# Optimization experiments

Hardware: AMD Instinct MI355X
Metric: run time of the kernel (lower is better)

The kernel has to match this reference:

```python
import jax, jax.numpy as jnp
import numpy as np

DIM = 1024
D_STATE = 16
D_CONV = 4
EXPAND = 2
D_INNER = EXPAND * DIM          # 2048
DT_RANK = -(-DIM // 16)        # ceil(dim/16) = 64
BATCH = 2
SEQ = 1024


def activation_quant(x):
    # int8 fake-quant with STE, per-row scale (matches torch source incl. grad paths)
    scale = 127.0 / jnp.clip(jnp.max(jnp.abs(x), axis=-1, keepdims=True), 1e-5)
    s = x * scale
    q = jnp.clip(jnp.round(s), -128.0, 127.0)
    return (jax.lax.stop_gradient(q - s) + s) / scale


def weight_quant(w):
    # ternary quant {-1,0,1} with straight-through estimator (grad = identity)
    scale = jnp.clip(jnp.mean(jnp.abs(w)), 1e-5)
    wq = jnp.clip(jnp.round(w / scale), -1.0, 1.0)
    return w + jax.lax.stop_gradient(wq - w)


def bit_linear(x, w):
    # LayerNorm (no affine, eps=1e-5) -> act quant -> ternary-weight matmul
    mu = jnp.mean(x, axis=-1, keepdims=True)
    var = jnp.mean((x - mu) ** 2, axis=-1, keepdims=True)
    xn = (x - mu) * jax.lax.rsqrt(var + 1e-5)
    return activation_quant(xn) @ weight_quant(w).T


def rms_norm(x, w, eps=1e-6):
    return w * (x * jax.lax.rsqrt(jnp.mean(x * x, axis=-1, keepdims=True) + eps))


def selective_scan(x, delta, A, Bm, Cm, D, z):
    # x, delta: [b,l,d]; Bm, Cm: [b,l,n]; A: [d,n]; D: [d]; z: [b,l,d]
    def step(h, inp):
        x_t, d_t, B_t, C_t = inp              # [b,d],[b,d],[b,n],[b,n]
        dA = jnp.exp(d_t[:, :, None] * A)     # [b,d,n]
        h = dA * h + d_t[:, :, None] * B_t[:, None, :] * x_t[:, :, None]
        y = jnp.einsum('bdn,bn->bd', h, C_t)
        return h, y

    h0 = jnp.zeros((x.shape[0], A.shape[0], A.shape[1]), x.dtype)
    seq_first = lambda t: jnp.moveaxis(t, 1, 0)
    _, ys = jax.lax.scan(step, h0, (seq_first(x), seq_first(delta), seq_first(Bm), seq_first(Cm)))
    y = jnp.moveaxis(ys, 0, 1) + x * D
    return y * jax.nn.silu(z)


def mamba_forward(hidden_states, rms_w, in_proj_w, x_proj_w, out_proj_w,
                  conv_w, conv_b, dt_proj_w, dt_proj_b, A_log, D):
    b, l, _ = hidden_states.shape
    h = rms_norm(hidden_states, rms_w)
    xz = bit_linear(h, in_proj_w)                      # [b,l,2*d_inner]
    x, z = jnp.split(xz, 2, axis=-1)

    # depthwise causal conv1d + bias
    xc = jnp.moveaxis(x, 1, 2)                         # [b,d_inner,l]
    xc = jax.lax.conv_general_dilated(
        xc, conv_w, window_strides=(1,), padding=[(D_CONV - 1, 0)],
        feature_group_count=D_INNER, dimension_numbers=('NCH', 'OIH', 'NCH'))
    xc = xc + conv_b[None, :, None]
    x = jax.nn.silu(jnp.moveaxis(xc, 1, 2))            # [b,l,d_inner]

    x_dbl = bit_linear(x, x_proj_w)                    # [b,l,dt_rank+2*d_state]
    dt_low, Bm, Cm = jnp.split(x_dbl, [DT_RANK, DT_RANK + D_STATE], axis=-1)
    dt = dt_low @ dt_proj_w.T + dt_proj_b              # dt_proj (with bias)
    # source passes dt_bias=dt_proj.bias again into the fused scan with softplus
    delta = jax.nn.softplus(dt + dt_proj_b)
    A = -jnp.exp(A_log)

    y = selective_scan(x, delta, A, Bm, Cm, D, z)
    out = bit_linear(y, out_proj_w)
    return hidden_states + out


def setup_inputs() -> dict:
    key = jax.random.key(0)
    ks = jax.random.split(key, 8)
    return {
        'hidden_states': jax.random.normal(ks[0], (BATCH, SEQ, DIM), jnp.float32),
        'rms_w': jnp.ones((DIM,), jnp.float32),
        'in_proj_w': jax.random.normal(ks[1], (2 * D_INNER, DIM), jnp.float32) / np.float32(np.sqrt(DIM)),
        'x_proj_w': jax.random.normal(ks[2], (DT_RANK + 2 * D_STATE, D_INNER), jnp.float32) / np.float32(np.sqrt(D_INNER)),
        'out_proj_w': jax.random.normal(ks[3], (DIM, D_INNER), jnp.float32) / np.float32(np.sqrt(D_INNER)),
        'conv_w': jax.random.normal(ks[4], (D_INNER, 1, D_CONV), jnp.float32) * 0.2,
        'conv_b': jnp.zeros((D_INNER,), jnp.float32),
        'dt_proj_w': jax.random.normal(ks[5], (D_INNER, DT_RANK), jnp.float32) / np.float32(np.sqrt(DT_RANK)),
        'dt_proj_b': jax.random.normal(ks[6], (D_INNER,), jnp.float32) * 0.01,
        'A_log': jnp.log(jnp.tile(jnp.arange(1, D_STATE + 1, dtype=jnp.float32), (D_INNER, 1))),
        'D': jnp.ones((D_INNER,), jnp.float32),
    }


def reference(hidden_states, rms_w, in_proj_w, x_proj_w, out_proj_w,
              conv_w, conv_b, dt_proj_w, dt_proj_b, A_log, D):
    return mamba_forward(hidden_states, rms_w, in_proj_w, x_proj_w, out_proj_w,
                         conv_w, conv_b, dt_proj_w, dt_proj_b, A_log, D)
```

## Files before the change

kernel.cpp:

```cpp
#include <hip/hip_runtime.h>
#include <hip/hip_bf16.h>

#define BATCH 2
#define SEQ 1024
#define DIM 1024
#define DINNER 2048
#define NSTATE 16
#define DTRANK 64
#define NDBL 96
#define ROWS (BATCH*SEQ)
#define NC 32
#define TC 32
#define KSPLIT 8

#define N_IN_W  (4096*1024)
#define N_X_W   (NDBL*DINNER)
#define N_OUT_W (1024*2048)

typedef __attribute__((ext_vector_type(8))) short bf16x8;
typedef __attribute__((ext_vector_type(4))) float f32x4;

__device__ inline float wave_sum64(float v){
#pragma unroll
  for (int o=32;o>0;o>>=1) v += __shfl_xor(v,o,64);
  return v;
}
__device__ inline float wave_max64(float v){
#pragma unroll
  for (int o=32;o>0;o>>=1) v = fmaxf(v,__shfl_xor(v,o,64));
  return v;
}
__device__ inline float block_sum256(float v, float* sred){
  v = wave_sum64(v);
  if ((threadIdx.x&63)==0) sred[threadIdx.x>>6]=v;
  __syncthreads();
  float t = sred[0]+sred[1]+sred[2]+sred[3];
  __syncthreads();
  return t;
}
__device__ inline float block_max256(float v, float* sred){
  v = wave_max64(v);
  if ((threadIdx.x&63)==0) sred[threadIdx.x>>6]=v;
  __syncthreads();
  float t = fmaxf(fmaxf(sred[0],sred[1]),fmaxf(sred[2],sred[3]));
  __syncthreads();
  return t;
}

__global__ __launch_bounds__(256) void absmean3_partial_k(const float* __restrict__ w0,
    const float* __restrict__ w1, const float* __restrict__ w2, float* __restrict__ part){
  __shared__ float sred[4];
  const float* w; int n;
  if (blockIdx.y==0){ w=w0; n=N_IN_W; }
  else if (blockIdx.y==1){ w=w1; n=N_X_W; }
  else { w=w2; n=N_OUT_W; }
  float s = 0.f;
  for (int i = blockIdx.x*256 + threadIdx.x; i < n; i += 512*256) s += fabsf(w[i]);
  s = block_sum256(s, sred);
  if (threadIdx.x==0) part[blockIdx.y*512 + blockIdx.x] = s;
}
__global__ __launch_bounds__(256) void absmean3_final_k(const float* __restrict__ part,
                                                        float* __restrict__ out){
  __shared__ float sred[4];
  const float cnt0 = (float)N_IN_W, cnt1 = (float)N_X_W, cnt2 = (float)N_OUT_W;
#pragma unroll
  for (int w=0; w<3; w++){
    float s = part[w*512 + threadIdx.x] + part[w*512 + threadIdx.x + 256];
    s = block_sum256(s, sred);
    if (threadIdx.x==0){
      const float c = (w==0)?cnt0:((w==1)?cnt1:cnt2);
      out[w] = fmaxf(s/c, 1e-5f);
    }
  }
}
__device__ inline void tern4(const float* __restrict__ w, ushort* __restrict__ wq,
                             int i, float s){
  const float4 v = ((const float4*)w)[i];
  float q0 = fminf(fmaxf(rintf(v.x/s),-1.f),1.f);
  float q1 = fminf(fmaxf(rintf(v.y/s),-1.f),1.f);
  float q2 = fminf(fmaxf(rintf(v.z/s),-1.f),1.f);
  float q3 = fminf(fmaxf(rintf(v.w/s),-1.f),1.f);
  __hip_bfloat16 h0=__float2bfloat16(q0), h1=__float2bfloat16(q1);
  __hip_bfloat16 h2=__float2bfloat16(q2), h3=__float2bfloat16(q3);
  ushort4 o;
  o.x=*(ushort*)&h0; o.y=*(ushort*)&h1; o.z=*(ushort*)&h2; o.w=*(ushort*)&h3;
  ((ushort4*)wq)[i]=o;
}
__global__ __launch_bounds__(256) void ternarize3_k(const float* __restrict__ w0,
    const float* __restrict__ w1, const float* __restrict__ w2,
    ushort* __restrict__ q0, ushort* __restrict__ q1, ushort* __restrict__ q2,
    const float* __restrict__ wsc){
  const int NQ0 = N_IN_W/4, NQ1 = N_X_W/4, PQ1 = (128*2048 - N_X_W)/4, NQ2 = N_OUT_W/4;
  int i = blockIdx.x*256 + threadIdx.x;
  if (i < NQ0){ tern4(w0, q0, i, wsc[0]); return; }
  i -= NQ0;
  if (i < NQ1){ tern4(w1, q1, i, wsc[1]); return; }
  i -= NQ1;
  if (i < PQ1){ ((ushort4*)q1)[NQ1 + i] = (ushort4){0,0,0,0}; return; }
  i -= PQ1;
  if (i < NQ2){ tern4(w2, q2, i, wsc[2]); }
}

template<int NV>
__global__ __launch_bounds__(256) void ln_quant_k(const float* __restrict__ src,
    const float* __restrict__ rmsw, __hip_bfloat16* __restrict__ q, float* __restrict__ rs){
  constexpr int C = NV*256;
  __shared__ float sred[4];
  const int r = blockIdx.x, tid = threadIdx.x;
  const float* row = src + (size_t)r*C;
  float v[NV];
#pragma unroll
  for (int i=0;i<NV;i++) v[i] = row[tid + i*256];
  if (rmsw){
    float ss=0.f;
#pragma unroll
    for (int i=0;i<NV;i++) ss += v[i]*v[i];
    ss = block_sum256(ss, sred);
    float f = rsqrtf(ss/(float)C + 1e-6f);
#pragma unroll
    for (int i=0;i<NV;i++) v[i] *= f * rmsw[tid + i*256];
  }
  float s=0.f;
#pragma unroll
  for (int i=0;i<NV;i++) s += v[i];
  s = block_sum256(s, sred);
  const float mu = s/(float)C;
  float vs=0.f;
#pragma unroll
  for (int i=0;i<NV;i++){ float d=v[i]-mu; vs += d*d; }
  vs = block_sum256(vs, sred);
  const float inv = rsqrtf(vs/(float)C + 1e-5f);
  float am=0.f;
#pragma unroll
  for (int i=0;i<NV;i++){ v[i] = (v[i]-mu)*inv; am = fmaxf(am, fabsf(v[i])); }
  am = block_max256(am, sred);
  am = fmaxf(am, 1e-5f);
  const float scale = 127.f/am;
  if (tid==0) rs[r] = am*(1.f/127.f);
#pragma unroll
  for (int i=0;i<NV;i++){
    float qv = fminf(fmaxf(rintf(v[i]*scale), -128.f), 127.f);
    q[(size_t)r*C + tid + i*256] = __float2bfloat16(qv);
  }
}

__global__ __launch_bounds__(256) void conv_ln_quant_k(const float* __restrict__ x,
    const float* __restrict__ cw, const float* __restrict__ cb,
    float* __restrict__ xc, __hip_bfloat16* __restrict__ q, float* __restrict__ rs){
  __shared__ float sred[4];
  const int r = blockIdx.x, tid = threadIdx.x;
  const int t = r & (SEQ-1);
  float v[8];
#pragma unroll
  for (int i=0;i<8;i++){
    const int d = tid + i*256;
    const float4 w4 = ((const float4*)cw)[d];
    const float wj[4] = {w4.x, w4.y, w4.z, w4.w};
    float acc = cb[d];
#pragma unroll
    for (int j=0;j<4;j++){
      const int tt = t-3+j;
      if (tt>=0) acc += x[(size_t)(r-3+j)*DINNER + d]*wj[j];
    }
    acc = acc/(1.f+expf(-acc));
    xc[(size_t)r*DINNER + d] = acc;
    v[i] = acc;
  }
  float s=0.f;
#pragma unroll
  for (int i=0;i<8;i++) s += v[i];
  s = block_sum256(s, sred);
  const float mu = s/2048.f;
  float vs=0.f;
#pragma unroll
  for (int i=0;i<8;i++){ float d=v[i]-mu; vs += d*d; }
  vs = block_sum256(vs, sred);
  const float inv = rsqrtf(vs/2048.f + 1e-5f);
  float am=0.f;
#pragma unroll
  for (int i=0;i<8;i++){ v[i] = (v[i]-mu)*inv; am = fmaxf(am, fabsf(v[i])); }
  am = block_max256(am, sred);
  am = fmaxf(am, 1e-5f);
  const float scale = 127.f/am;
  if (tid==0) rs[r] = am*(1.f/127.f);
#pragma unroll
  for (int i=0;i<8;i++){
    float qv = fminf(fmaxf(rintf(v[i]*scale), -128.f), 127.f);
    q[(size_t)r*2048 + tid + i*256] = __float2bfloat16(qv);
  }
}

template<int BM, int BN, int MODE>
__global__ __launch_bounds__(256) void gemm2_k(
    const short* __restrict__ A, const short* __restrict__ Bw,
    const float* __restrict__ rs, int K, int Ksub, int ldc,
    float* __restrict__ out0, float* __restrict__ out1,
    const float* __restrict__ hid)
{
  constexpr int MF = BM/32;
  constexpr int NF = BN/32;
  constexpr int CA = BM/32;
  constexpr int CB = BN/32;
  __shared__ short lsA[BM*64];
  __shared__ short lsB[BN*64];
  const int tid = threadIdx.x;
  const int w = tid>>6, l = tid&63;
  const int m0 = blockIdx.x*BM, n0 = blockIdx.y*BN;
  const int wr = (w>>1)*(BM/2), wc = (w&1)*(BN/2);
  const int lr = l&15, g = l>>4;
  f32x4 acc[MF][NF];
#pragma unroll
  for (int m=0;m<MF;m++)
#pragma unroll
    for (int n=0;n<NF;n++) acc[m][n] = (f32x4){0.f,0.f,0.f,0.f};

  const size_t KB = (size_t)K*2;
  const char* Ag = (const char*)A + (size_t)m0*KB + (size_t)blockIdx.z*Ksub*2;
  const char* Bg = (const char*)Bw + (size_t)n0*KB + (size_t)blockIdx.z*Ksub*2;

  bf16x8 ra[CA], rb[CB];
#define LDG(kb)                                                                   \
  {                                                                               \
    _Pragma("unroll")                                                             \
    for (int c=0;c<CA;c++){ int o=c*4096+tid*16; int rw=o>>7, cl=o&127;           \
      ra[c] = *(const bf16x8*)(Ag + (size_t)rw*KB + (size_t)(kb)*2 + cl); }       \
    _Pragma("unroll")                                                             \
    for (int c=0;c<CB;c++){ int o=c*4096+tid*16; int rw=o>>7, cl=o&127;           \
      rb[c] = *(const bf16x8*)(Bg + (size_t)rw*KB + (size_t)(kb)*2 + cl); }       \
  }

  LDG(0);
  for (int kb=0; kb<Ksub; kb+=64){
    __syncthreads();
#pragma unroll
    for (int c=0;c<CA;c++){ int o=c*4096+tid*16; int rw=o>>7, sl=(o>>4)&7;
      *(bf16x8*)((char*)lsA + (rw<<7) + ((sl^(rw&7))<<4)) = ra[c]; }
#pragma unroll
    for (int c=0;c<CB;c++){ int o=c*4096+tid*16; int rw=o>>7, sl=(o>>4)&7;
      *(bf16x8*)((char*)lsB + (rw<<7) + ((sl^(rw&7))<<4)) = rb[c]; }
    __syncthreads();
    if (kb + 64 < Ksub) LDG(kb+64);
#pragma unroll
    for (int ks=0;ks<2;ks++){
      bf16x8 af[MF], bb[NF];
#pragma unroll
      for (int m=0;m<MF;m++){ int rw = wr + m*16 + lr;
        af[m] = *(const bf16x8*)((const char*)lsA + (rw<<7) + ((((ks<<2)+g)^(lr&7))<<4)); }
#pragma unroll
      for (int n=0;n<NF;n++){ int rw = wc + n*16 + lr;
        bb[n] = *(const bf16x8*)((const char*)lsB + (rw<<7) + ((((ks<<2)+g)^(lr&7))<<4)); }
#pragma unroll
      for (int m=0;m<MF;m++)
#pragma unroll
        for (int n=0;n<NF;n++)
          acc[m][n] = __builtin_amdgcn_mfma_f32_16x16x32_bf16(af[m], bb[n], acc[m][n], 0, 0, 0);
    }
  }
#undef LDG

#pragma unroll
  for (int m=0;m<MF;m++){
    const int rowb = m0 + wr + m*16 + g*4;
#pragma unroll
    for (int j=0;j<4;j++){
      const int row = rowb + j;
      const float rsv = (MODE==3) ? 1.f : rs[row];
#pragma unroll
      for (int n=0;n<NF;n++){
        const int col = n0 + wc + n*16 + lr;
        const float v = acc[m][n][j]*rsv;
        if (MODE==1){
          if (col < 2048) out0[(size_t)row*2048 + col] = v;
          else            out1[(size_t)row*2048 + (col-2048)] = v;
        } else if (MODE==2){
          const size_t o = (size_t)row*ldc + col;
          out0[o] = hid[o] + v;
        } else {
          out0[((size_t)blockIdx.z*2048 + row)*128 + col] = v;
        }
      }
    }
  }
}

__global__ __launch_bounds__(256) void xproj_combine_k(const float* __restrict__ part,
    const float* __restrict__ rs, float* __restrict__ xdbl){
  const int idx = blockIdx.x*256 + threadIdx.x;
  const int row = idx/NDBL, c = idx - row*NDBL;
  float s = 0.f;
#pragma unroll
  for (int z=0; z<KSPLIT; z++) s += part[((size_t)z*ROWS + row)*128 + c];
  xdbl[(size_t)idx] = s * rs[row];
}

#define SXT_S 130
#define SW2_S 66
__global__ __launch_bounds__(256) void dt_delta2_k(const float* __restrict__ xdbl,
    const float* __restrict__ W, const float* __restrict__ bias, float* __restrict__ delta){
  __shared__ float sXT[64*SXT_S];
  __shared__ float sW2[64*SW2_S];
  const int tid = threadIdx.x;
  const int r0 = blockIdx.x*128, d0 = blockIdx.y*64;
#pragma unroll
  for (int qit=0;qit<8;qit++){
    const int f4 = qit*256 + tid;
    const int rr = f4>>4, k0 = (f4&15)<<2;
    const float4 xv4 = *(const float4*)(xdbl + (size_t)(r0+rr)*NDBL + k0);
    sXT[(k0+0)*SXT_S + rr] = xv4.x;
    sXT[(k0+1)*SXT_S + rr] = xv4.y;
    sXT[(k0+2)*SXT_S + rr] = xv4.z;
    sXT[(k0+3)*SXT_S + rr] = xv4.w;
  }
#pragma unroll
  for (int qit=0;qit<4;qit++){
    const int f4 = qit*256 + tid;
    const int dd = f4>>4, k0 = (f4&15)<<2;
    const float4 wv4 = *(const float4*)(W + (size_t)(d0+dd)*64 + k0);
    sW2[(k0+0)*SW2_S + dd] = wv4.x;
    sW2[(k0+1)*SW2_S + dd] = wv4.y;
    sW2[(k0+2)*SW2_S + dd] = wv4.z;
    sW2[(k0+3)*SW2_S + dd] = wv4.w;
  }
  __syncthreads();
  const int tx = tid&15, ty = tid>>4;
  float acc[8][4];
#pragma unroll
  for (int i=0;i<8;i++)
#pragma unroll
    for (int j=0;j<4;j++) acc[i][j]=0.f;
  for (int k=0;k<64;k++){
    float xv[8], wv[4];
    *(float2*)&xv[0] = *(const float2*)&sXT[k*SXT_S + ty*8 + 0];
    *(float2*)&xv[2] = *(const float2*)&sXT[k*SXT_S + ty*8 + 2];
    *(float2*)&xv[4] = *(const float2*)&sXT[k*SXT_S + ty*8 + 4];
    *(float2*)&xv[6] = *(const float2*)&sXT[k*SXT_S + ty*8 + 6];
    *(float2*)&wv[0] = *(const float2*)&sW2[k*SW2_S + tx*4 + 0];
    *(float2*)&wv[2] = *(const float2*)&sW2[k*SW2_S + tx*4 + 2];
#pragma unroll
    for (int i=0;i<8;i++)
#pragma unroll
      for (int j=0;j<4;j++) acc[i][j] = fmaf(xv[i], wv[j], acc[i][j]);
  }
  const float4 b4 = *(const float4*)(bias + d0 + tx*4);
  const float b2[4] = {2.f*b4.x, 2.f*b4.y, 2.f*b4.z, 2.f*b4.w};
#pragma unroll
  for (int i=0;i<8;i++){
    const int row = r0 + ty*8 + i;
    float4 o;
    float* op = (float*)&o;
#pragma unroll
    for (int j=0;j<4;j++){
      const float xq = acc[i][j] + b2[j];
      op[j] = (xq>20.f) ? xq : log1pf(expf(xq));
    }
    *(float4*)(delta + (size_t)row*DINNER + d0 + tx*4) = o;
  }
}

__global__ __launch_bounds__(256) void scan1_k(const float* __restrict__ delta,
    const float* __restrict__ xc, const float* __restrict__ xdbl,
    const float* __restrict__ A_log, float* __restrict__ hloc, float* __restrict__ Ssum){
  __shared__ float sB[TC][16];
  const int tid = threadIdx.x;
  const int d = blockIdx.x*256 + tid;
  const int c = blockIdx.y, b = blockIdx.z;
  const int row0 = b*SEQ + c*TC;
  for (int i=tid;i<TC*16;i+=256){
    int t=i>>4, j=i&15;
    sB[t][j] = xdbl[(size_t)(row0+t)*NDBL + DTRANK + j];
  }
  __syncthreads();
  float a[16];
  const f32x4* Ap = (const f32x4*)(A_log + (size_t)d*16);
#pragma unroll
  for (int q=0;q<4;q++){
    f32x4 av = Ap[q];
#pragma unroll
    for (int j=0;j<4;j++) a[q*4+j] = -__expf(av[j]);
  }
  float h[16];
#pragma unroll
  for (int n=0;n<16;n++) h[n]=0.f;
  float S = 0.f;
  float dl = delta[(size_t)row0*DINNER + d];
  float xv = xc[(size_t)row0*DINNER + d];
  for (int t=0;t<TC;t++){
    const float dlc=dl, xvc=xv;
    if (t<TC-1){
      dl = delta[(size_t)(row0+t+1)*DINNER + d];
      xv = xc[(size_t)(row0+t+1)*DINNER + d];
    }
    S += dlc;
    const float dx = dlc*xvc;
#pragma unroll
    for (int n=0;n<16;n++)
      h[n] = fmaf(__expf(dlc*a[n]), h[n], dx*sB[t][n]);
  }
  f32x4* hp = (f32x4*)(hloc + ((size_t)(b*NC+c)*DINNER + d)*16);
#pragma unroll
  for (int q=0;q<4;q++){
    f32x4 hv;
#pragma unroll
    for (int j=0;j<4;j++) hv[j]=h[q*4+j];
    hp[q]=hv;
  }
  Ssum[(size_t)(b*NC+c)*DINNER + d] = S;
}

__global__ __launch_bounds__(256) void scan2_k(const float* __restrict__ A_log,
    const float* __restrict__ Ssum, float* __restrict__ hloc){
  const int idx = blockIdx.x*256 + threadIdx.x;
  const int n = idx&15, d = (idx>>4)&(DINNER-1), b = idx>>15;
  const float a = -__expf(A_log[(size_t)d*16+n]);
  float hin = 0.f;
  for (int c=0;c<NC;c++){
    const size_t o = ((size_t)(b*NC+c)*DINNER + d)*16 + n;
    const float t = hloc[o];
    hloc[o] = hin;
    hin = fmaf(__expf(a*Ssum[(size_t)(b*NC+c)*DINNER + d]), hin, t);
  }
}

__global__ __launch_bounds__(256) void scan3_k(const float* __restrict__ delta,
    const float* __restrict__ xc, const float* __restrict__ xdbl,
    const float* __restrict__ A_log, const float* __restrict__ Dp,
    const float* __restrict__ hloc, float* __restrict__ zy){
  __shared__ float sBC[TC][32];
  const int tid = threadIdx.x;
  const int d = blockIdx.x*256 + tid;
  const int c = blockIdx.y, b = blockIdx.z;
  const int row0 = b*SEQ + c*TC;
  for (int i=tid;i<TC*32;i+=256){
    int t=i>>5, j=i&31;
    sBC[t][j] = xdbl[(size_t)(row0+t)*NDBL + DTRANK + j];
  }
  __syncthreads();
  float a[16];
  const f32x4* Ap = (const f32x4*)(A_log + (size_t)d*16);
#pragma unroll
  for (int q=0;q<4;q++){
    f32x4 av = Ap[q];
#pragma unroll
    for (int j=0;j<4;j++) a[q*4+j] = -__expf(av[j]);
  }
  float h[16];
  const f32x4* hp = (const f32x4*)(hloc + ((size_t)(b*NC+c)*DINNER + d)*16);
#pragma unroll
  for (int q=0;q<4;q++){
    f32x4 hv = hp[q];
#pragma unroll
    for (int j=0;j<4;j++) h[q*4+j]=hv[j];
  }
  const float Dv = Dp[d];
  float dl = delta[(size_t)row0*DINNER + d];
  float xv = xc[(size_t)row0*DINNER + d];
  float zv = zy[(size_t)row0*DINNER + d];
  for (int t=0;t<TC;t++){
    const float dlc=dl, xvc=xv, zvc=zv;
    if (t<TC-1){
      dl = delta[(size_t)(row0+t+1)*DINNER + d];
      xv = xc[(size_t)(row0+t+1)*DINNER + d];
      zv = zy[(size_t)(row0+t+1)*DINNER + d];
    }
    const float dx = dlc*xvc;
    float p = 0.f;
#pragma unroll
    for (int n=0;n<16;n++){
      h[n] = fmaf(__expf(dlc*a[n]), h[n], dx*sBC[t][n]);
      p = fmaf(h[n], sBC[t][16+n], p);
    }
    float y = p + xvc*Dv;
    y *= zvc/(1.f+__expf(-zvc));
    zy[(size_t)(row0+t)*DINNER + d] = y;
  }
}

extern "C" void kernel_launch(void* const* d_in, const int* in_sizes, int n_in,
                              void* d_out, int out_size, void* d_ws, size_t ws_size,
                              hipStream_t stream){
  (void)in_sizes; (void)n_in; (void)out_size; (void)ws_size;
  const float* hidden    = (const float*)d_in[0];
  const float* rms_w     = (const float*)d_in[1];
  const float* in_proj_w = (const float*)d_in[2];
  const float* x_proj_w  = (const float*)d_in[3];
  const float* out_proj_w= (const float*)d_in[4];
  const float* conv_w    = (const float*)d_in[5];
  const float* conv_b    = (const float*)d_in[6];
  const float* dt_proj_w = (const float*)d_in[7];
  const float* dt_proj_b = (const float*)d_in[8];
  const float* A_log     = (const float*)d_in[9];
  const float* Dp        = (const float*)d_in[10];

  char* ws = (char*)d_ws; size_t off = 0;
  auto alloc = [&](size_t b)->void* { void* p = ws + off; off += (b + 255) & ~(size_t)255; return p; };
  float* part3 = (float*)alloc(3*512*4);
  float* wsc   = (float*)alloc(256);
  float* RS    = (float*)alloc((size_t)ROWS*4);
  __hip_bfloat16* WQin  = (__hip_bfloat16*)alloc((size_t)4096*1024*2);
  __hip_bfloat16* WQx   = (__hip_bfloat16*)alloc((size_t)128*2048*2);
  __hip_bfloat16* WQout = (__hip_bfloat16*)alloc((size_t)1024*2048*2);
  __hip_bfloat16* QA    = (__hip_bfloat16*)alloc((size_t)ROWS*2048*2);
  float* XBUF  = (float*)alloc((size_t)ROWS*DINNER*4);
  float* ZBUF  = (float*)alloc((size_t)ROWS*DINNER*4);
  float* XC    = (float*)alloc((size_t)ROWS*DINNER*4);
  float* XDBL  = (float*)alloc((size_t)ROWS*NDBL*4);
  float* HLOC  = (float*)alloc((size_t)BATCH*NC*DINNER*16*4);
  float* SSUM  = (float*)alloc((size_t)BATCH*NC*DINNER*4);
  float* XPART = (float*)alloc((size_t)KSPLIT*ROWS*128*4);

  absmean3_partial_k<<<dim3(512,3),256,0,stream>>>(in_proj_w, x_proj_w, out_proj_w, part3);
  absmean3_final_k<<<1,256,0,stream>>>(part3, wsc);
  {
    const int totq = N_IN_W/4 + 128*2048/4 + N_OUT_W/4;
    ternarize3_k<<<(totq+255)/256,256,0,stream>>>(in_proj_w, x_proj_w, out_proj_w,
        (ushort*)WQin, (ushort*)WQx, (ushort*)WQout, wsc);
  }

  ln_quant_k<4><<<ROWS,256,0,stream>>>(hidden, rms_w, QA, RS);
  gemm2_k<128,128,1><<<dim3(ROWS/128, 4096/128, 1),256,0,stream>>>((const short*)QA,
      (const short*)WQin, RS, DIM, DIM, 0, XBUF, ZBUF, nullptr);
  conv_ln_quant_k<<<ROWS,256,0,stream>>>(XBUF, conv_w, conv_b, XC, QA, RS);
  gemm2_k<64,128,3><<<dim3(ROWS/64, 1, KSPLIT),256,0,stream>>>((const short*)QA,
      (const short*)WQx, nullptr, DINNER, DINNER/KSPLIT, 0, XPART, nullptr, nullptr);
  xproj_combine_k<<<(ROWS*NDBL)/256,256,0,stream>>>(XPART, RS, XDBL);
  dt_delta2_k<<<dim3(ROWS/128, DINNER/64),256,0,stream>>>(XDBL, dt_proj_w, dt_proj_b, XBUF);
  scan1_k<<<dim3(DINNER/256, NC, BATCH),256,0,stream>>>(XBUF, XC, XDBL, A_log, HLOC, SSUM);
  scan2_k<<<(BATCH*DINNER*16)/256,256,0,stream>>>(A_log, SSUM, HLOC);
  scan3_k<<<dim3(DINNER/256, NC, BATCH),256,0,stream>>>(XBUF, XC, XDBL, A_log, Dp, HLOC, ZBUF);
  ln_quant_k<8><<<ROWS,256,0,stream>>>(ZBUF, nullptr, QA, RS);
  gemm2_k<64,64,2><<<dim3(ROWS/64, 1024/64, 1),256,0,stream>>>((const short*)QA,
      (const short*)WQout, RS, DINNER, DINNER, DIM, (float*)d_out, nullptr, hidden);
}
```

Baseline: 181.3 us.

## Merge prelude kernels and replace split-K combine with atomic accumulation

The weight abs-mean partial sums, the first RMSNorm/LayerNorm quant pass and zeroing of the x_proj output now run in one prelude launch. The abs-mean finalization is recomputed per block inside the ternarize kernel, so the one-block final kernel is gone. The x_proj split-K GEMM accumulates directly into XDBL with atomicAdd, which removes the partial buffer and the combine kernel. The per-row scale is applied where XDBL is consumed (dt_delta, scan1, scan3). This trades fewer launches and less intermediate traffic for atomic contention, redundant per-block reductions, and non-deterministic summation order.

```diff
diff --git a/kernel.cpp b/kernel.cpp
--- a/kernel.cpp
+++ b/kernel.cpp
@@ -47,32 +47,70 @@
   return t;
 }
 
-__global__ __launch_bounds__(256) void absmean3_partial_k(const float* __restrict__ w0,
-    const float* __restrict__ w1, const float* __restrict__ w2, float* __restrict__ part){
+__global__ __launch_bounds__(256) void prelude_k(
+    const float* __restrict__ w0, const float* __restrict__ w1,
+    const float* __restrict__ w2, float* __restrict__ part,
+    const float* __restrict__ hidden, const float* __restrict__ rmsw,
+    __hip_bfloat16* __restrict__ q, float* __restrict__ rs,
+    float* __restrict__ xdbl_zero)
+{
   __shared__ float sred[4];
-  const float* w; int n;
-  if (blockIdx.y==0){ w=w0; n=N_IN_W; }
-  else if (blockIdx.y==1){ w=w1; n=N_X_W; }
-  else { w=w2; n=N_OUT_W; }
-  float s = 0.f;
-  for (int i = blockIdx.x*256 + threadIdx.x; i < n; i += 512*256) s += fabsf(w[i]);
-  s = block_sum256(s, sred);
-  if (threadIdx.x==0) part[blockIdx.y*512 + blockIdx.x] = s;
-}
-__global__ __launch_bounds__(256) void absmean3_final_k(const float* __restrict__ part,
-                                                        float* __restrict__ out){
-  __shared__ float sred[4];
-  const float cnt0 = (float)N_IN_W, cnt1 = (float)N_X_W, cnt2 = (float)N_OUT_W;
-#pragma unroll
-  for (int w=0; w<3; w++){
-    float s = part[w*512 + threadIdx.x] + part[w*512 + threadIdx.x + 256];
+  const int bid = blockIdx.x, tid = threadIdx.x;
+  if (bid < 1536){
+    const int wsel = bid >> 9, bx = bid & 511;
+    const float* w; int n;
+    if (wsel==0){ w=w0; n=N_IN_W; }
+    else if (wsel==1){ w=w1; n=N_X_W; }
+    else { w=w2; n=N_OUT_W; }
+    float s = 0.f;
+    for (int i = bx*256 + tid; i < n; i += 512*256) s += fabsf(w[i]);
     s = block_sum256(s, sred);
-    if (threadIdx.x==0){
-      const float c = (w==0)?cnt0:((w==1)?cnt1:cnt2);
-      out[w] = fmaxf(s/c, 1e-5f);
-    }
-  }
-}
+    if (tid==0) part[wsel*512 + bx] = s;
+    return;
+  }
+  if (bid < 3584){
+    const int r = bid - 1536;
+    const float* row = hidden + (size_t)r*1024;
+    float v[4];
+#pragma unroll
+    for (int i=0;i<4;i++) v[i] = row[tid + i*256];
+    float ss=0.f;
+#pragma unroll
+    for (int i=0;i<4;i++) ss += v[i]*v[i];
+    ss = block_sum256(ss, sred);
+    float f = rsqrtf(ss/1024.f + 1e-6f);
+#pragma unroll
+    for (int i=0;i<4;i++) v[i] *= f * rmsw[tid + i*256];
+    float s=0.f;
+#pragma unroll
+    for (int i=0;i<4;i++) s += v[i];
+    s = block_sum256(s, sred);
+    const float mu = s/1024.f;
+    float vs=0.f;
+#pragma unroll
+    for (int i=0;i<4;i++){ float d=v[i]-mu; vs += d*d; }
+    vs = block_sum256(vs, sred);
+    const float inv = rsqrtf(vs/1024.f + 1e-5f);
+    float am=0.f;
+#pragma unroll
+    for (int i=0;i<4;i++){ v[i] = (v[i]-mu)*inv; am = fmaxf(am, fabsf(v[i])); }
+    am = block_max256(am, sred);
+    am = fmaxf(am, 1e-5f);
+    const float scale = 127.f/am;
+    if (tid==0) rs[r] = am*(1.f/127.f);
+#pragma unroll
+    for (int i=0;i<4;i++){
+      float qv = fminf(fmaxf(rintf(v[i]*scale), -128.f), 127.f);
+      q[(size_t)r*1024 + tid + i*256] = __float2bfloat16(qv);
+    }
+    return;
+  }
+  {
+    const int idx = (bid - 3584)*256 + tid;
+    ((float4*)xdbl_zero)[idx] = (float4){0.f,0.f,0.f,0.f};
+  }
+}
+
 __device__ inline void tern4(const float* __restrict__ w, ushort* __restrict__ wq,
                              int i, float s){
   const float4 v = ((const float4*)w)[i];
@@ -86,62 +124,28 @@
   o.x=*(ushort*)&h0; o.y=*(ushort*)&h1; o.z=*(ushort*)&h2; o.w=*(ushort*)&h3;
   ((ushort4*)wq)[i]=o;
 }
-__global__ __launch_bounds__(256) void ternarize3_k(const float* __restrict__ w0,
+__global__ __launch_bounds__(256) void ternarize3b_k(const float* __restrict__ w0,
     const float* __restrict__ w1, const float* __restrict__ w2,
     ushort* __restrict__ q0, ushort* __restrict__ q1, ushort* __restrict__ q2,
-    const float* __restrict__ wsc){
+    const float* __restrict__ part){
+  __shared__ float sred[4];
+  float sc[3];
+#pragma unroll
+  for (int w=0; w<3; w++){
+    float s = part[w*512 + threadIdx.x] + part[w*512 + threadIdx.x + 256];
+    s = block_sum256(s, sred);
+    const float c = (w==0)?(float)N_IN_W:((w==1)?(float)N_X_W:(float)N_OUT_W);
+    sc[w] = fmaxf(s/c, 1e-5f);
+  }
   const int NQ0 = N_IN_W/4, NQ1 = N_X_W/4, PQ1 = (128*2048 - N_X_W)/4, NQ2 = N_OUT_W/4;
   int i = blockIdx.x*256 + threadIdx.x;
-  if (i < NQ0){ tern4(w0, q0, i, wsc[0]); return; }
+  if (i < NQ0){ tern4(w0, q0, i, sc[0]); return; }
   i -= NQ0;
-  if (i < NQ1){ tern4(w1, q1, i, wsc[1]); return; }
+  if (i < NQ1){ tern4(w1, q1, i, sc[1]); return; }
   i -= NQ1;
   if (i < PQ1){ ((ushort4*)q1)[NQ1 + i] = (ushort4){0,0,0,0}; return; }
   i -= PQ1;
-  if (i < NQ2){ tern4(w2, q2, i, wsc[2]); }
-}
-
-template<int NV>
-__global__ __launch_bounds__(256) void ln_quant_k(const float* __restrict__ src,
-    const float* __restrict__ rmsw, __hip_bfloat16* __restrict__ q, float* __restrict__ rs){
-  constexpr int C = NV*256;
-  __shared__ float sred[4];
-  const int r = blockIdx.x, tid = threadIdx.x;
-  const float* row = src + (size_t)r*C;
-  float v[NV];
-#pragma unroll
-  for (int i=0;i<NV;i++) v[i] = row[tid + i*256];
-  if (rmsw){
-    float ss=0.f;
-#pragma unroll
-    for (int i=0;i<NV;i++) ss += v[i]*v[i];
-    ss = block_sum256(ss, sred);
-    float f = rsqrtf(ss/(float)C + 1e-6f);
-#pragma unroll
-    for (int i=0;i<NV;i++) v[i] *= f * rmsw[tid + i*256];
-  }
-  float s=0.f;
-#pragma unroll
-  for (int i=0;i<NV;i++) s += v[i];
-  s = block_sum256(s, sred);
-  const float mu = s/(float)C;
-  float vs=0.f;
-#pragma unroll
-  for (int i=0;i<NV;i++){ float d=v[i]-mu; vs += d*d; }
-  vs = block_sum256(vs, sred);
-  const float inv = rsqrtf(vs/(float)C + 1e-5f);
-  float am=0.f;
-#pragma unroll
-  for (int i=0;i<NV;i++){ v[i] = (v[i]-mu)*inv; am = fmaxf(am, fabsf(v[i])); }
-  am = block_max256(am, sred);
-  am = fmaxf(am, 1e-5f);
-  const float scale = 127.f/am;
-  if (tid==0) rs[r] = am*(1.f/127.f);
-#pragma unroll
-  for (int i=0;i<NV;i++){
-    float qv = fminf(fmaxf(rintf(v[i]*scale), -128.f), 127.f);
-    q[(size_t)r*C + tid + i*256] = __float2bfloat16(qv);
-  }
+  if (i < NQ2){ tern4(w2, q2, i, sc[2]); }
 }
 
 __global__ __launch_bounds__(256) void conv_ln_quant_k(const float* __restrict__ x,
@@ -166,6 +170,38 @@
     xc[(size_t)r*DINNER + d] = acc;
     v[i] = acc;
   }
+  float s=0.f;
+#pragma unroll
+  for (int i=0;i<8;i++) s += v[i];
+  s = block_sum256(s, sred);
+  const float mu = s/2048.f;
+  float vs=0.f;
+#pragma unroll
+  for (int i=0;i<8;i++){ float d=v[i]-mu; vs += d*d; }
+  vs = block_sum256(vs, sred);
+  const float inv = rsqrtf(vs/2048.f + 1e-5f);
+  float am=0.f;
+#pragma unroll
+  for (int i=0;i<8;i++){ v[i] = (v[i]-mu)*inv; am = fmaxf(am, fabsf(v[i])); }
+  am = block_max256(am, sred);
+  am = fmaxf(am, 1e-5f);
+  const float scale = 127.f/am;
+  if (tid==0) rs[r] = am*(1.f/127.f);
+#pragma unroll
+  for (int i=0;i<8;i++){
+    float qv = fminf(fmaxf(rintf(v[i]*scale), -128.f), 127.f);
+    q[(size_t)r*2048 + tid + i*256] = __float2bfloat16(qv);
+  }
+}
+
+__global__ __launch_bounds__(256) void ln_quant8_k(const float* __restrict__ src,
+    __hip_bfloat16* __restrict__ q, float* __restrict__ rs){
+  __shared__ float sred[4];
+  const int r = blockIdx.x, tid = threadIdx.x;
+  const float* row = src + (size_t)r*2048;
+  float v[8];
+#pragma unroll
+  for (int i=0;i<8;i++) v[i] = row[tid + i*256];
   float s=0.f;
 #pragma unroll
   for (int i=0;i<8;i++) s += v[i];
@@ -264,7 +300,7 @@
 #pragma unroll
     for (int j=0;j<4;j++){
       const int row = rowb + j;
-      const float rsv = (MODE==3) ? 1.f : rs[row];
+      const float rsv = (MODE==4) ? 1.f : rs[row];
 #pragma unroll
       for (int n=0;n<NF;n++){
         const int col = n0 + wc + n*16 + lr;
@@ -276,26 +312,17 @@
           const size_t o = (size_t)row*ldc + col;
           out0[o] = hid[o] + v;
         } else {
-          out0[((size_t)blockIdx.z*2048 + row)*128 + col] = v;
+          if (col < NDBL) atomicAdd(&out0[(size_t)row*NDBL + col], v);
         }
       }
     }
   }
-}
-
-__global__ __launch_bounds__(256) void xproj_combine_k(const float* __restrict__ part,
-    const float* __restrict__ rs, float* __restrict__ xdbl){
-  const int idx = blockIdx.x*256 + threadIdx.x;
-  const int row = idx/NDBL, c = idx - row*NDBL;
-  float s = 0.f;
-#pragma unroll
-  for (int z=0; z<KSPLIT; z++) s += part[((size_t)z*ROWS + row)*128 + c];
-  xdbl[(size_t)idx] = s * rs[row];
 }
 
 #define SXT_S 130
 #define SW2_S 66
 __global__ __launch_bounds__(256) void dt_delta2_k(const float* __restrict__ xdbl,
+    const float* __restrict__ rs,
     const float* __restrict__ W, const float* __restrict__ bias, float* __restrict__ delta){
   __shared__ float sXT[64*SXT_S];
   __shared__ float sW2[64*SW2_S];
@@ -305,11 +332,12 @@
   for (int qit=0;qit<8;qit++){
     const int f4 = qit*256 + tid;
     const int rr = f4>>4, k0 = (f4&15)<<2;
+    const float rsv = rs[r0+rr];
     const float4 xv4 = *(const float4*)(xdbl + (size_t)(r0+rr)*NDBL + k0);
-    sXT[(k0+0)*SXT_S + rr] = xv4.x;
-    sXT[(k0+1)*SXT_S + rr] = xv4.y;
-    sXT[(k0+2)*SXT_S + rr] = xv4.z;
-    sXT[(k0+3)*SXT_S + rr] = xv4.w;
+    sXT[(k0+0)*SXT_S + rr] = xv4.x*rsv;
+    sXT[(k0+1)*SXT_S + rr] = xv4.y*rsv;
+    sXT[(k0+2)*SXT_S + rr] = xv4.z*rsv;
+    sXT[(k0+3)*SXT_S + rr] = xv4.w*rsv;
   }
 #pragma unroll
   for (int qit=0;qit<4;qit++){
@@ -359,6 +387,7 @@
 
 __global__ __launch_bounds__(256) void scan1_k(const float* __restrict__ delta,
     const float* __restrict__ xc, const float* __restrict__ xdbl,
+    const float* __restrict__ rs,
     const float* __restrict__ A_log, float* __restrict__ hloc, float* __restrict__ Ssum){
   __shared__ float sB[TC][16];
   const int tid = threadIdx.x;
@@ -367,7 +396,7 @@
   const int row0 = b*SEQ + c*TC;
   for (int i=tid;i<TC*16;i+=256){
     int t=i>>4, j=i&15;
-    sB[t][j] = xdbl[(size_t)(row0+t)*NDBL + DTRANK + j];
+    sB[t][j] = xdbl[(size_t)(row0+t)*NDBL + DTRANK + j] * rs[row0+t];
   }
   __syncthreads();
   float a[16];
@@ -423,6 +452,7 @@
 
 __global__ __launch_bounds__(256) void scan3_k(const float* __restrict__ delta,
     const float* __restrict__ xc, const float* __restrict__ xdbl,
+    const float* __restrict__ rs,
     const float* __restrict__ A_log, const float* __restrict__ Dp,
     const float* __restrict__ hloc, float* __restrict__ zy){
   __shared__ float sBC[TC][32];
@@ -432,7 +462,7 @@
   const int row0 = b*SEQ + c*TC;
   for (int i=tid;i<TC*32;i+=256){
     int t=i>>5, j=i&31;
-    sBC[t][j] = xdbl[(size_t)(row0+t)*NDBL + DTRANK + j];
+    sBC[t][j] = xdbl[(size_t)(row0+t)*NDBL + DTRANK + j] * rs[row0+t];
   }
   __syncthreads();
   float a[16];
@@ -494,7 +524,6 @@
   char* ws = (char*)d_ws; size_t off = 0;
   auto alloc = [&](size_t b)->void* { void* p = ws + off; off += (b + 255) & ~(size_t)255; return p; };
   float* part3 = (float*)alloc(3*512*4);
-  float* wsc   = (float*)alloc(256);
   float* RS    = (float*)alloc((size_t)ROWS*4);
   __hip_bfloat16* WQin  = (__hip_bfloat16*)alloc((size_t)4096*1024*2);
   __hip_bfloat16* WQx   = (__hip_bfloat16*)alloc((size_t)128*2048*2);
@@ -506,28 +535,24 @@
   float* XDBL  = (float*)alloc((size_t)ROWS*NDBL*4);
   float* HLOC  = (float*)alloc((size_t)BATCH*NC*DINNER*16*4);
   float* SSUM  = (float*)alloc((size_t)BATCH*NC*DINNER*4);
-  float* XPART = (float*)alloc((size_t)KSPLIT*ROWS*128*4);
-
-  absmean3_partial_k<<<dim3(512,3),256,0,stream>>>(in_proj_w, x_proj_w, out_proj_w, part3);
-  absmean3_final_k<<<1,256,0,stream>>>(part3, wsc);
+
+  prelude_k<<<3776,256,0,stream>>>(in_proj_w, x_proj_w, out_proj_w, part3,
+                                   hidden, rms_w, QA, RS, XDBL);
   {
     const int totq = N_IN_W/4 + 128*2048/4 + N_OUT_W/4;
-    ternarize3_k<<<(totq+255)/256,256,0,stream>>>(in_proj_w, x_proj_w, out_proj_w,
-        (ushort*)WQin, (ushort*)WQx, (ushort*)WQout, wsc);
-  }
-
-  ln_quant_k<4><<<ROWS,256,0,stream>>>(hidden, rms_w, QA, RS);
+    ternarize3b_k<<<(totq+255)/256,256,0,stream>>>(in_proj_w, x_proj_w, out_proj_w,
+        (ushort*)WQin, (ushort*)WQx, (ushort*)WQout, part3);
+  }
   gemm2_k<128,128,1><<<dim3(ROWS/128, 4096/128, 1),256,0,stream>>>((const short*)QA,
       (const short*)WQin, RS, DIM, DIM, 0, XBUF, ZBUF, nullptr);
   conv_ln_quant_k<<<ROWS,256,0,stream>>>(XBUF, conv_w, conv_b, XC, QA, RS);
-  gemm2_k<64,128,3><<<dim3(ROWS/64, 1, KSPLIT),256,0,stream>>>((const short*)QA,
-      (const short*)WQx, nullptr, DINNER, DINNER/KSPLIT, 0, XPART, nullptr, nullptr);
-  xproj_combine_k<<<(ROWS*NDBL)/256,256,0,stream>>>(XPART, RS, XDBL);
-  dt_delta2_k<<<dim3(ROWS/128, DINNER/64),256,0,stream>>>(XDBL, dt_proj_w, dt_proj_b, XBUF);
-  scan1_k<<<dim3(DINNER/256, NC, BATCH),256,0,stream>>>(XBUF, XC, XDBL, A_log, HLOC, SSUM);
+  gemm2_k<64,128,4><<<dim3(ROWS/64, 1, KSPLIT),256,0,stream>>>((const short*)QA,
+      (const short*)WQx, nullptr, DINNER, DINNER/KSPLIT, NDBL, XDBL, nullptr, nullptr);
+  dt_delta2_k<<<dim3(ROWS/128, DINNER/64),256,0,stream>>>(XDBL, RS, dt_proj_w, dt_proj_b, XBUF);
+  scan1_k<<<dim3(DINNER/256, NC, BATCH),256,0,stream>>>(XBUF, XC, XDBL, RS, A_log, HLOC, SSUM);
   scan2_k<<<(BATCH*DINNER*16)/256,256,0,stream>>>(A_log, SSUM, HLOC);
-  scan3_k<<<dim3(DINNER/256, NC, BATCH),256,0,stream>>>(XBUF, XC, XDBL, A_log, Dp, HLOC, ZBUF);
-  ln_quant_k<8><<<ROWS,256,0,stream>>>(ZBUF, nullptr, QA, RS);
+  scan3_k<<<dim3(DINNER/256, NC, BATCH),256,0,stream>>>(XBUF, XC, XDBL, RS, A_log, Dp, HLOC, ZBUF);
+  ln_quant8_k<<<ROWS,256,0,stream>>>(ZBUF, QA, RS);
   gemm2_k<64,64,2><<<dim3(ROWS/64, 1024/64, 1),256,0,stream>>>((const short*)QA,
       (const short*)WQout, RS, DINNER, DINNER, DIM, (float*)d_out, nullptr, hidden);
 }
```

Result: no change. 180.1 us (-0.6%).
